# Optimization experiments

Hardware: AMD Instinct MI355X
Metric: run time of the kernel (lower is better)

## Reference

```python
import jax, jax.numpy as jnp
import numpy as np

B, T, HID, NH = 8, 4096, 768, 12
HD = HID // NH          # 64
WIN = 128 // 2          # half window = 64 (local_attention=128)
BLK = 64                # block size == half window
THETA = 10000.0         # local_rope_theta
ATTN_SCALING = 1.0      # default rope type


def setup_inputs() -> dict:
    key = jax.random.key(0)
    k1, k2, k3 = jax.random.split(key, 3)
    hidden_states = jax.random.normal(k1, (B, T, HID), jnp.float32)
    attention_mask = jnp.ones((B, T), jnp.bool_)
    Wqkv = jax.random.normal(k2, (3 * HID, HID), jnp.float32) * 0.02
    Wo = jax.random.normal(k3, (HID, HID), jnp.float32) * 0.02
    return {"hidden_states": hidden_states, "attention_mask": attention_mask,
            "Wqkv": Wqkv, "Wo": Wo}


def _rope(x):
    # x: [B, T, NH, HD]; interleaved-pair complex rotation (pairs = reshape(HD//2, 2))
    pos = jnp.arange(T, dtype=jnp.float32)
    inv_freq = 1.0 / (THETA ** (jnp.arange(0, HD, 2, dtype=jnp.float32) / HD))  # [HD/2]
    ang = pos[:, None] * inv_freq[None, :]                 # [T, HD/2]
    cos = jnp.cos(ang)[None, :, None, :]
    sin = jnp.sin(ang)[None, :, None, :]
    pairs = x.reshape(x.shape[:-1] + (HD // 2, 2))
    a, b = pairs[..., 0], pairs[..., 1]
    ra = a * cos - b * sin
    rb = a * sin + b * cos
    return (jnp.stack([ra, rb], axis=-1).reshape(x.shape)) * ATTN_SCALING


def reference(hidden_states, attention_mask, Wqkv, Wo):
    # fused QKV projection (no bias: attention_bias=False)
    qkv = hidden_states @ Wqkv.T                            # [B, T, 3*HID]
    qkv = qkv.reshape(B, T, 3, NH, HD)
    q, k, v = qkv[:, :, 0], qkv[:, :, 1], qkv[:, :, 2]      # [B, T, NH, HD]
    q = _rope(q)
    k = _rope(k)

    # Blocked sliding-window attention: block = 64, each query block attends
    # key blocks {i-1, i, i+1}; exact +/-64 band enforced by mask.
    nb = T // BLK
    pad = [(0, 0), (BLK, BLK), (0, 0), (0, 0)]
    kp = jnp.pad(k, pad)
    vp = jnp.pad(v, pad)
    kb = kp.reshape(B, nb + 2, BLK, NH, HD)
    vb = vp.reshape(B, nb + 2, BLK, NH, HD)
    knb = jnp.concatenate([kb[:, :-2], kb[:, 1:-1], kb[:, 2:]], axis=2)  # [B, nb, 3*BLK, NH, HD]
    vnb = jnp.concatenate([vb[:, :-2], vb[:, 1:-1], vb[:, 2:]], axis=2)
    qb = q.reshape(B, nb, BLK, NH, HD)

    scores = jnp.einsum('bnqhd,bnkhd->bhnqk', qb, knb) / jnp.sqrt(jnp.float32(HD))
    band = jnp.abs(BLK + jnp.arange(BLK)[:, None] - jnp.arange(3 * BLK)[None, :]) <= WIN  # [BLK, 3*BLK]
    mp = jnp.pad(attention_mask.astype(jnp.bool_), [(0, 0), (BLK, BLK)])
    mb = mp.reshape(B, nb + 2, BLK)
    mnb = jnp.concatenate([mb[:, :-2], mb[:, 1:-1], mb[:, 2:]], axis=2)  # [B, nb, 3*BLK]
    mask = band[None, None, None] & mnb[:, None, :, None, :]
    scores = jnp.where(mask, scores, -jnp.inf)
    probs = jax.nn.softmax(scores, axis=-1)
    out = jnp.einsum('bhnqk,bnkhd->bnqhd', probs, vnb)      # [B, nb, BLK, NH, HD]
    out = out.reshape(B, T, HID)
    return out @ Wo.T
```

## Files before the change

### kernel.cpp

```cpp
#include <hip/hip_runtime.h>
#include <hip/hip_bf16.h>

#define T_SEQ 4096
#define NH 12

typedef __bf16 bf16x8 __attribute__((ext_vector_type(8)));
typedef float f32x4 __attribute__((ext_vector_type(4)));
typedef unsigned int uint32;

__device__ __forceinline__ void gload_lds16(const void* g, void* lds) {
    __builtin_amdgcn_global_load_lds((const __attribute__((address_space(1))) void*)g,
                                     (__attribute__((address_space(3))) void*)lds,
                                     16, 0, 0);
}

__device__ __forceinline__ f32x4 mfma16(bf16x8 a, bf16x8 b, f32x4 c) {
    return __builtin_amdgcn_mfma_f32_16x16x32_bf16(a, b, c, 0, 0, 0);
}

__device__ __forceinline__ void store_out(__hip_bfloat16* p, float v) { *p = __float2bfloat16(v); }
__device__ __forceinline__ void store_out(float* p, float v) { *p = v; }

__global__ __launch_bounds__(256) void f32_to_bf16_kernel(const float* __restrict__ src,
                                                          __hip_bfloat16* __restrict__ dst,
                                                          long n8) {
    long i = (long)blockIdx.x * 256 + threadIdx.x;
    if (i >= n8) return;
    float4 a = *(const float4*)(src + i * 8);
    float4 b = *(const float4*)(src + i * 8 + 4);
    __hip_bfloat16 o[8];
    o[0] = __float2bfloat16(a.x); o[1] = __float2bfloat16(a.y);
    o[2] = __float2bfloat16(a.z); o[3] = __float2bfloat16(a.w);
    o[4] = __float2bfloat16(b.x); o[5] = __float2bfloat16(b.y);
    o[6] = __float2bfloat16(b.z); o[7] = __float2bfloat16(b.w);
    *(uint4*)(dst + i * 8) = *(uint4*)o;
}

__global__ void rope_table_kernel(float2* __restrict__ tab) {
    int idx = blockIdx.x * 256 + threadIdx.x;
    int tpos = idx >> 5, i = idx & 31;
    float invf = powf(10000.0f, -(2.0f * i) / 64.0f);
    float ang = (float)tpos * invf;
    tab[idx] = make_float2((float)cos((double)ang), (float)sin((double)ang));
}

template <typename OutT>
__global__ __launch_bounds__(256) void gemm_nt(const __hip_bfloat16* __restrict__ A,
                                               const __hip_bfloat16* __restrict__ Bw,
                                               OutT* __restrict__ C,
                                               int M, int N, int K, int nbn) {
    __shared__ __align__(16) __hip_bfloat16 As[128 * 64];
    __shared__ __align__(16) __hip_bfloat16 Bs[128 * 64];
    const int tid = threadIdx.x;
    const int w = tid >> 6, l = tid & 63;
    const int g = l >> 4, li = l & 15;
    const int wr = w >> 1, wc = w & 1;

    const int cpx = gridDim.x >> 3;
    const int bid = blockIdx.x;
    const int swz = (bid & 7) * cpx + (bid >> 3);
    const int bm = swz / nbn, bn = swz % nbn;

    const long abase = (long)bm * 128 * K;
    const long bbase = (long)bn * 128 * K;

    f32x4 acc[4][4] = {};

    for (int k0 = 0; k0 < K; k0 += 64) {
#pragma unroll
        for (int i = 0; i < 4; ++i) {
            int seg = i * 256 + tid;
            int row = seg >> 3;
            int chunk = seg & 7;
            int schunk = chunk ^ (row & 7);
            int segb = i * 256 + (tid & ~63);
            gload_lds16(A + abase + (long)row * K + k0 + schunk * 8, (char*)As + (size_t)segb * 16);
            gload_lds16(Bw + bbase + (long)row * K + k0 + schunk * 8, (char*)Bs + (size_t)segb * 16);
        }
        __syncthreads();
#pragma unroll
        for (int kk = 0; kk < 64; kk += 32) {
            bf16x8 af[4], bfr[4];
#pragma unroll
            for (int mi = 0; mi < 4; ++mi) {
                const int row = wr * 64 + mi * 16 + li;
                const int gc = (kk >> 3) + g;
                af[mi] = *(const bf16x8*)((char*)As + row * 128 + ((gc ^ (row & 7)) << 4));
            }
#pragma unroll
            for (int ni = 0; ni < 4; ++ni) {
                const int row = wc * 64 + ni * 16 + li;
                const int gc = (kk >> 3) + g;
                bfr[ni] = *(const bf16x8*)((char*)Bs + row * 128 + ((gc ^ (row & 7)) << 4));
            }
#pragma unroll
            for (int mi = 0; mi < 4; ++mi)
#pragma unroll
                for (int ni = 0; ni < 4; ++ni)
                    acc[mi][ni] = mfma16(af[mi], bfr[ni], acc[mi][ni]);
        }
        __syncthreads();
    }

#pragma unroll
    for (int mi = 0; mi < 4; ++mi)
#pragma unroll
        for (int ni = 0; ni < 4; ++ni)
#pragma unroll
            for (int r = 0; r < 4; ++r) {
                long row = (long)bm * 128 + wr * 64 + mi * 16 + g * 4 + r;
                int col = bn * 128 + wc * 64 + ni * 16 + li;
                store_out(&C[row * (long)N + col], acc[mi][ni][r]);
            }
}

__global__ __launch_bounds__(256) void attn_kernel(const __hip_bfloat16* __restrict__ qkv,
                                                   __hip_bfloat16* __restrict__ attn_out,
                                                   const float2* __restrict__ tab) {
    __shared__ __align__(16) char smem[51200];
    __hip_bfloat16* Qs = (__hip_bfloat16*)smem;
    __hip_bfloat16* Ks = (__hip_bfloat16*)(smem + 9216);
    __hip_bfloat16* Ps = (__hip_bfloat16*)smem;
    __hip_bfloat16* Vs = (__hip_bfloat16*)(smem + 25600);

    const int tid = threadIdx.x;
    const int w = tid >> 6, l = tid & 63;
    const int g = l >> 4, li = l & 15;
    const int mw = w * 16;

    const int bid = blockIdx.x;
    const int n = bid & 63;
    const int bh = bid >> 6;
    const int b = bh / NH, h = bh % NH;

    const long tokq0 = (long)b * T_SEQ + n * 64;
    const long rowbase = (long)b * T_SEQ;

#pragma unroll
    for (int i = 0; i < 2; ++i) {
        int seg = i * 256 + tid;
        int row = seg >> 3, c = (seg & 7) * 8;
        uint4 v = *(const uint4*)&qkv[(tokq0 + row) * 2304 + h * 64 + c];
        __hip_bfloat16 tmp[8], outv[8];
        *(uint4*)tmp = v;
        const int tpos = n * 64 + row;
#pragma unroll
        for (int j = 0; j < 4; ++j) {
            float2 cs = tab[tpos * 32 + (c >> 1) + j];
            float a = __bfloat162float(tmp[2 * j]), bb = __bfloat162float(tmp[2 * j + 1]);
            outv[2 * j]     = __float2bfloat16(a * cs.x - bb * cs.y);
            outv[2 * j + 1] = __float2bfloat16(a * cs.y + bb * cs.x);
        }
        *(uint4*)&Qs[row * 72 + c] = *(uint4*)outv;
    }
#pragma unroll
    for (int i = 0; i < 6; ++i) {
        int seg = i * 256 + tid;
        int row = seg >> 3, c = (seg & 7) * 8;
        int tk = n * 64 - 64 + row;
        tk = tk < 0 ? 0 : (tk > T_SEQ - 1 ? T_SEQ - 1 : tk);
        uint4 v = *(const uint4*)&qkv[(rowbase + tk) * 2304 + 768 + h * 64 + c];
        __hip_bfloat16 tmp[8], outv[8];
        *(uint4*)tmp = v;
#pragma unroll
        for (int j = 0; j < 4; ++j) {
            float2 cs = tab[tk * 32 + (c >> 1) + j];
            float a = __bfloat162float(tmp[2 * j]), bb = __bfloat162float(tmp[2 * j + 1]);
            outv[2 * j]     = __float2bfloat16(a * cs.x - bb * cs.y);
            outv[2 * j + 1] = __float2bfloat16(a * cs.y + bb * cs.x);
        }
        *(uint4*)&Ks[row * 72 + c] = *(uint4*)outv;
    }
    __syncthreads();

    f32x4 s[12] = {};
#pragma unroll
    for (int kk = 0; kk < 64; kk += 32) {
        bf16x8 aq = *(const bf16x8*)&Qs[(mw + li) * 72 + kk + g * 8];
#pragma unroll
        for (int ni = 0; ni < 12; ++ni) {
            bf16x8 bk = *(const bf16x8*)&Ks[(ni * 16 + li) * 72 + kk + g * 8];
            s[ni] = mfma16(aq, bk, s[ni]);
        }
    }

#pragma unroll
    for (int r = 0; r < 4; ++r) {
        int q = mw + g * 4 + r;
        float mx = -1e30f;
#pragma unroll
        for (int ni = 0; ni < 12; ++ni) {
            int k = ni * 16 + li;
            int kpos = n * 64 - 64 + k;
            bool valid = (k >= q) && (k <= q + 128) && (kpos >= 0) && (kpos < T_SEQ);
            float v = valid ? s[ni][r] * 0.125f : -1e30f;
            s[ni][r] = v;
            mx = fmaxf(mx, v);
        }
#pragma unroll
        for (int m = 1; m < 16; m <<= 1) mx = fmaxf(mx, __shfl_xor(mx, m, 64));
        float sum = 0.f;
#pragma unroll
        for (int ni = 0; ni < 12; ++ni) {
            float e = __expf(s[ni][r] - mx);
            s[ni][r] = e;
            sum += e;
        }
#pragma unroll
        for (int m = 1; m < 16; m <<= 1) sum += __shfl_xor(sum, m, 64);
        float inv = 1.0f / sum;
#pragma unroll
        for (int ni = 0; ni < 12; ++ni) s[ni][r] *= inv;
    }
    __syncthreads();

#pragma unroll
    for (int r = 0; r < 4; ++r) {
        int q = mw + g * 4 + r;
#pragma unroll
        for (int ni = 0; ni < 12; ++ni)
            Ps[q * 200 + ni * 16 + li] = __float2bfloat16(s[ni][r]);
    }
#pragma unroll
    for (int i = 0; i < 6; ++i) {
        int seg = i * 256 + tid;
        int row = seg >> 3, c = (seg & 7) * 8;
        int tk = n * 64 - 64 + row;
        tk = tk < 0 ? 0 : (tk > T_SEQ - 1 ? T_SEQ - 1 : tk);
        uint4 v = *(const uint4*)&qkv[(rowbase + tk) * 2304 + 1536 + h * 64 + c];
        __hip_bfloat16 tmp[8];
        *(uint4*)tmp = v;
#pragma unroll
        for (int j = 0; j < 8; ++j) Vs[(c + j) * 200 + row] = tmp[j];
    }
    __syncthreads();

    f32x4 o[4] = {};
#pragma unroll
    for (int kk = 0; kk < 192; kk += 32) {
        bf16x8 ap = *(const bf16x8*)&Ps[(mw + li) * 200 + kk + g * 8];
#pragma unroll
        for (int ni = 0; ni < 4; ++ni) {
            bf16x8 bv = *(const bf16x8*)&Vs[(ni * 16 + li) * 200 + kk + g * 8];
            o[ni] = mfma16(ap, bv, o[ni]);
        }
    }
#pragma unroll
    for (int ni = 0; ni < 4; ++ni)
#pragma unroll
        for (int r = 0; r < 4; ++r) {
            int q = mw + g * 4 + r;
            attn_out[(tokq0 + q) * 768 + h * 64 + ni * 16 + li] = __float2bfloat16(o[ni][r]);
        }
}

extern "C" void kernel_launch(void* const* d_in, const int* in_sizes, int n_in,
                              void* d_out, int out_size, void* d_ws, size_t ws_size,
                              hipStream_t stream) {
    const float* hidden = (const float*)d_in[0];
    const float* Wqkv = (const float*)d_in[2];
    const float* Wo   = (const float*)d_in[3];
    float* out = (float*)d_out;

    char* ws = (char*)d_ws;
    __hip_bfloat16* qkv     = (__hip_bfloat16*)ws;
    __hip_bfloat16* abuf    = (__hip_bfloat16*)(ws + 150994944L);
    __hip_bfloat16* wqkv_bf = (__hip_bfloat16*)(ws + 201326592L);
    __hip_bfloat16* wo_bf   = (__hip_bfloat16*)(ws + 204865536L);
    float2*         tab     = (float2*)(ws + 206045184L);

    f32_to_bf16_kernel<<<12288, 256, 0, stream>>>(hidden, abuf, 3145728);
    f32_to_bf16_kernel<<<864, 256, 0, stream>>>(Wqkv, wqkv_bf, 221184);
    f32_to_bf16_kernel<<<288, 256, 0, stream>>>(Wo, wo_bf, 73728);
    rope_table_kernel<<<512, 256, 0, stream>>>(tab);

    gemm_nt<__hip_bfloat16><<<4608, 256, 0, stream>>>(abuf, wqkv_bf, qkv, 32768, 2304, 768, 18);
    attn_kernel<<<6144, 256, 0, stream>>>(qkv, abuf, tab);
    gemm_nt<float><<<1536, 256, 0, stream>>>(abuf, wo_bf, out, 32768, 768, 768, 6);
}
```

Measured before the change: 329.5 us.

## Replace GEMM with 256x256-tile 8-wave double-buffered pipelined kernel

Swaps the single-buffered 128x128 GEMM for a 512-thread kernel with 256x256 output tiles. It double-buffers the LDS and splits each K-step into four phases that interleave half-tile global-to-LDS loads with MFMA work, using explicit vmcnt waits, barriers and setprio. Larger tiles raise arithmetic intensity and the prefetching hides load latency, at the cost of 128KB LDS and higher register pressure. Grid counts shrink (1152 and 384 blocks), which may underfill 256 CUs, especially for the output projection.

Result: slower. 349.7 us (+6.1%).

```diff
diff --git a/kernel.cpp b/kernel.cpp
--- a/kernel.cpp
+++ b/kernel.cpp
@@ -44,72 +44,122 @@
     tab[idx] = make_float2((float)cos((double)ang), (float)sin((double)ang));
 }
 
+
+#define PHASE(BB, MH, NH, SKIND, SKT, DOSTAGE)                                            \
+    do {                                                                                  \
+        bf16x8 af[4][2], bq[2][2];                                                        \
+        _Pragma("unroll")                                                                 \
+        for (int m2 = 0; m2 < 4; ++m2)                                                    \
+            _Pragma("unroll")                                                             \
+            for (int ks = 0; ks < 2; ++ks) {                                              \
+                const int row = wr * 128 + ((MH) * 4 + m2) * 16 + li;                     \
+                af[m2][ks] = *(const bf16x8*)((char*)&As[BB][0] + row * 128 +             \
+                                              (((ks * 4 + g) ^ (row & 7)) << 4));         \
+            }                                                                             \
+        _Pragma("unroll")                                                                 \
+        for (int n2 = 0; n2 < 2; ++n2)                                                    \
+            _Pragma("unroll")                                                             \
+            for (int ks = 0; ks < 2; ++ks) {                                              \
+                const int row = wc * 64 + ((NH) * 2 + n2) * 16 + li;                      \
+                bq[n2][ks] = *(const bf16x8*)((char*)&Bs[BB][0] + row * 128 +             \
+                                              (((ks * 4 + g) ^ (row & 7)) << 4));         \
+            }                                                                             \
+        if (DOSTAGE) STAGE_HT((SKIND), (SKT));                                            \
+        __builtin_amdgcn_sched_barrier(0);                                                \
+        __builtin_amdgcn_s_barrier();                                                     \
+        __builtin_amdgcn_s_setprio(1);                                                    \
+        _Pragma("unroll")                                                                 \
+        for (int m2 = 0; m2 < 4; ++m2)                                                    \
+            _Pragma("unroll")                                                             \
+            for (int n2 = 0; n2 < 2; ++n2)                                                \
+                _Pragma("unroll")                                                         \
+                for (int ks = 0; ks < 2; ++ks)                                            \
+                    acc[(MH) * 4 + m2][(NH) * 2 + n2] =                                   \
+                        mfma16(af[m2][ks], bq[n2][ks], acc[(MH) * 4 + m2][(NH) * 2 + n2]);\
+        __builtin_amdgcn_s_setprio(0);                                                    \
+        __builtin_amdgcn_sched_barrier(0);                                                \
+    } while (0)
+
 template <typename OutT>
-__global__ __launch_bounds__(256) void gemm_nt(const __hip_bfloat16* __restrict__ A,
-                                               const __hip_bfloat16* __restrict__ Bw,
-                                               OutT* __restrict__ C,
-                                               int M, int N, int K, int nbn) {
-    __shared__ __align__(16) __hip_bfloat16 As[128 * 64];
-    __shared__ __align__(16) __hip_bfloat16 Bs[128 * 64];
+__global__ __launch_bounds__(512) void gemm8p(const __hip_bfloat16* __restrict__ A,
+                                              const __hip_bfloat16* __restrict__ Bw,
+                                              OutT* __restrict__ C,
+                                              int M, int N, int K, int nbn) {
+    __shared__ __align__(16) __hip_bfloat16 As[2][256 * 64];
+    __shared__ __align__(16) __hip_bfloat16 Bs[2][256 * 64];
+
     const int tid = threadIdx.x;
     const int w = tid >> 6, l = tid & 63;
     const int g = l >> 4, li = l & 15;
-    const int wr = w >> 1, wc = w & 1;
+    const int wr = w >> 2, wc = w & 3;
 
     const int cpx = gridDim.x >> 3;
     const int bid = blockIdx.x;
     const int swz = (bid & 7) * cpx + (bid >> 3);
     const int bm = swz / nbn, bn = swz % nbn;
 
-    const long abase = (long)bm * 128 * K;
-    const long bbase = (long)bn * 128 * K;
-
-    f32x4 acc[4][4] = {};
-
-    for (int k0 = 0; k0 < K; k0 += 64) {
-#pragma unroll
-        for (int i = 0; i < 4; ++i) {
-            int seg = i * 256 + tid;
-            int row = seg >> 3;
-            int chunk = seg & 7;
-            int schunk = chunk ^ (row & 7);
-            int segb = i * 256 + (tid & ~63);
-            gload_lds16(A + abase + (long)row * K + k0 + schunk * 8, (char*)As + (size_t)segb * 16);
-            gload_lds16(Bw + bbase + (long)row * K + k0 + schunk * 8, (char*)Bs + (size_t)segb * 16);
-        }
-        __syncthreads();
-#pragma unroll
-        for (int kk = 0; kk < 64; kk += 32) {
-            bf16x8 af[4], bfr[4];
-#pragma unroll
-            for (int mi = 0; mi < 4; ++mi) {
-                const int row = wr * 64 + mi * 16 + li;
-                const int gc = (kk >> 3) + g;
-                af[mi] = *(const bf16x8*)((char*)As + row * 128 + ((gc ^ (row & 7)) << 4));
+    const long abase = (long)bm * 256 * K;
+    const long bbase = (long)bn * 256 * K;
+    const int NT = K >> 6;
+
+    auto STAGE_HT = [&](int kind, int kt) {
+        const int sb = kt & 1;
+        const int k0 = kt << 6;
+#pragma unroll
+        for (int i = 0; i < 2; ++i) {
+            const int ci = i * 512 + tid;
+            const int ir = ci >> 3;
+            const int ch = ci & 7;
+            const int ir0 = (i * 512 + (tid & ~63)) >> 3;
+            int row, row0;
+            if (kind < 2) {
+                row  = (ir & 63) + ((ir >> 6) << 7) + ((kind & 1) << 6);
+                row0 = (ir0 & 63) + ((ir0 >> 6) << 7) + ((kind & 1) << 6);
+            } else {
+                row  = (ir & 31) + ((ir >> 5) << 6) + ((kind & 1) << 5);
+                row0 = (ir0 & 31) + ((ir0 >> 5) << 6) + ((kind & 1) << 5);
             }
-#pragma unroll
-            for (int ni = 0; ni < 4; ++ni) {
-                const int row = wc * 64 + ni * 16 + li;
-                const int gc = (kk >> 3) + g;
-                bfr[ni] = *(const bf16x8*)((char*)Bs + row * 128 + ((gc ^ (row & 7)) << 4));
-            }
-#pragma unroll
-            for (int mi = 0; mi < 4; ++mi)
-#pragma unroll
-                for (int ni = 0; ni < 4; ++ni)
-                    acc[mi][ni] = mfma16(af[mi], bfr[ni], acc[mi][ni]);
-        }
-        __syncthreads();
-    }
-
-#pragma unroll
-    for (int mi = 0; mi < 4; ++mi)
+            const int sch = ch ^ (row & 7);
+            if (kind < 2)
+                gload_lds16(A + abase + (long)row * K + k0 + sch * 8,
+                            (char*)&As[sb][0] + (size_t)row0 * 128);
+            else
+                gload_lds16(Bw + bbase + (long)row * K + k0 + sch * 8,
+                            (char*)&Bs[sb][0] + (size_t)row0 * 128);
+        }
+    };
+
+    f32x4 acc[8][4] = {};
+
+    STAGE_HT(0, 0); STAGE_HT(2, 0); STAGE_HT(1, 0); STAGE_HT(3, 0);
+    STAGE_HT(2, 1); STAGE_HT(0, 1);
+    asm volatile("s_waitcnt vmcnt(4)" ::: "memory");
+    __builtin_amdgcn_s_barrier();
+
+    for (int j = 0; j < NT; ++j) {
+        const int bb = j & 1;
+        PHASE(bb, 0, 0, 1, j + 1, j + 1 < NT);
+        __builtin_amdgcn_s_barrier();
+        PHASE(bb, 1, 0, 3, j + 1, j + 1 < NT);
+        __builtin_amdgcn_s_barrier();
+        PHASE(bb, 0, 1, 2, j + 2, j + 2 < NT);
+        __builtin_amdgcn_s_barrier();
+        PHASE(bb, 1, 1, 0, j + 2, j + 2 < NT);
+        if (j + 1 < NT) {
+            if (j + 2 < NT) asm volatile("s_waitcnt vmcnt(4)" ::: "memory");
+            else            asm volatile("s_waitcnt vmcnt(0)" ::: "memory");
+        }
+        __builtin_amdgcn_s_barrier();
+    }
+
+#pragma unroll
+    for (int mi = 0; mi < 8; ++mi)
 #pragma unroll
         for (int ni = 0; ni < 4; ++ni)
 #pragma unroll
             for (int r = 0; r < 4; ++r) {
-                long row = (long)bm * 128 + wr * 64 + mi * 16 + g * 4 + r;
-                int col = bn * 128 + wc * 64 + ni * 16 + li;
+                long row = (long)bm * 256 + wr * 128 + mi * 16 + g * 4 + r;
+                int col = bn * 256 + wc * 64 + ni * 16 + li;
                 store_out(&C[row * (long)N + col], acc[mi][ni][r]);
             }
 }
@@ -274,7 +324,7 @@
     f32_to_bf16_kernel<<<288, 256, 0, stream>>>(Wo, wo_bf, 73728);
     rope_table_kernel<<<512, 256, 0, stream>>>(tab);
 
-    gemm_nt<__hip_bfloat16><<<4608, 256, 0, stream>>>(abuf, wqkv_bf, qkv, 32768, 2304, 768, 18);
+    gemm8p<__hip_bfloat16><<<1152, 512, 0, stream>>>(abuf, wqkv_bf, qkv, 32768, 2304, 768, 9);
     attn_kernel<<<6144, 256, 0, stream>>>(qkv, abuf, tab);
-    gemm_nt<float><<<1536, 256, 0, stream>>>(abuf, wo_bf, out, 32768, 768, 768, 6);
-}
+    gemm8p<float><<<384, 512, 0, stream>>>(abuf, wo_bf, out, 32768, 768, 768, 3);
+}
```
